# Performance work log

Hardware: AMD Instinct MI355X
Metric: run time of the kernel (lower is better)

## Reference

```python
import jax, jax.numpy as jnp
import numpy as np

EPS_NORM = 1e-12  # F.normalize eps
EPS_LN = 1e-5     # LayerNorm eps
TEMP = 0.1


def _l2norm(v, axis=-1):
    n = jnp.linalg.norm(v, axis=axis, keepdims=True)
    return v / jnp.maximum(n, EPS_NORM)


def setup_inputs() -> dict:
    key = jax.random.key(0)
    ks = jax.random.split(key, 6)
    B, D, P = 65536, 1024, 32
    x = jax.random.normal(ks[0], (B, D), dtype=jnp.float32)
    Wi = jax.random.normal(ks[1], (D, D), dtype=jnp.float32) * 0.02
    bi = jnp.zeros((D,), dtype=jnp.float32)
    Wo = jax.random.normal(ks[2], (D, 2 * D), dtype=jnp.float32) * 0.02
    bo = jnp.zeros((D,), dtype=jnp.float32)
    gamma = jnp.ones((D,), dtype=jnp.float32)
    beta = jnp.zeros((D,), dtype=jnp.float32)
    prototypes = _l2norm(jax.random.normal(ks[3], (P, D), dtype=jnp.float32))
    return {"x": x, "Wi": Wi, "bi": bi, "Wo": Wo, "bo": bo,
            "gamma": gamma, "beta": beta, "prototypes": prototypes}


def reference(x, Wi, bi, Wo, bo, gamma, beta, prototypes):
    # h = in_proj(x)
    h = x @ Wi.T + bi                      # [B, D]
    h_norm = _l2norm(h)
    proto_norm = _l2norm(prototypes)       # [P, D]
    sim = (h_norm @ proto_norm.T) / TEMP   # [B, P]
    attn = jax.nn.softmax(sim, axis=-1)
    retrieved = attn @ prototypes          # [B, D]
    combined = jnp.concatenate([x, retrieved], axis=-1)  # [B, 2D]
    out = jax.nn.gelu(combined @ Wo.T + bo, approximate=False)
    # dropout is identity in eval mode
    y = out + x
    mu = jnp.mean(y, axis=-1, keepdims=True)
    var = jnp.var(y, axis=-1, keepdims=True)
    return (y - mu) * jax.lax.rsqrt(var + EPS_LN) * gamma + beta
```

## Files before the change

### kernel.cpp

```cpp
#include <hip/hip_runtime.h>
#include <hip/hip_bf16.h>
#include <math.h>

typedef unsigned short u16;
typedef __attribute__((ext_vector_type(8))) short bf16x8;
typedef __attribute__((ext_vector_type(4))) float f32x4;
typedef __attribute__((address_space(1))) unsigned int gu32;
typedef __attribute__((address_space(3))) unsigned int lu32;

#define DD 1024
#define PP 32

__device__ __forceinline__ u16 f2bf(float f) {
  unsigned u = __float_as_uint(f);
  unsigned r = u + 0x7fffu + ((u >> 16) & 1u);
  return (u16)(r >> 16);
}
__device__ __forceinline__ float bf2f(u16 h) {
  return __uint_as_float(((unsigned)h) << 16);
}

__device__ __forceinline__ float gelu_t(float v) {
  float u = v + 0.044715f * v * v * v;
  float p = __builtin_amdgcn_exp2f(2.302590614f * u);
  float th = 1.0f - 2.0f * __builtin_amdgcn_rcpf(p + 1.0f);
  return 0.5f * v * (1.0f + th);
}

__global__ __launch_bounds__(256) void k_convert(const float* __restrict__ in,
                                                 u16* __restrict__ out, int n4) {
  for (int i = blockIdx.x * 256 + threadIdx.x; i < n4; i += gridDim.x * 256) {
    float4 v = ((const float4*)in)[i];
    ushort4 o;
    o.x = f2bf(v.x); o.y = f2bf(v.y); o.z = f2bf(v.z); o.w = f2bf(v.w);
    ((ushort4*)out)[i] = o;
  }
}

__global__ __launch_bounds__(256) void k_convert_wo(const float* __restrict__ Wo,
                                                    u16* __restrict__ WoB) {
  int i = blockIdx.x * 256 + threadIdx.x;
  int n = i >> 8, c4 = i & 255;
  float4 v = ((const float4*)(Wo + (size_t)n * 2048))[c4];
  ushort4 o;
  o.x = f2bf(v.x); o.y = f2bf(v.y); o.z = f2bf(v.z); o.w = f2bf(v.w);
  *(ushort4*)(WoB + (size_t)n * 1088 + c4 * 4) = o;
}

__global__ __launch_bounds__(256) void k_proto_prep(const float* __restrict__ protos,
                                                    u16* __restrict__ pb) {
  __shared__ float sb[4];
  int row = blockIdx.x, tid = threadIdx.x;
  float4 v = ((const float4*)(protos + row * DD))[tid];
  float q = v.x * v.x + v.y * v.y + v.z * v.z + v.w * v.w;
#pragma unroll
  for (int off = 32; off; off >>= 1) q += __shfl_xor(q, off);
  if ((tid & 63) == 0) sb[tid >> 6] = q;
  __syncthreads();
  q = sb[0] + sb[1] + sb[2] + sb[3];
  float inv = 1.0f / fmaxf(sqrtf(q), 1e-12f);
  ushort4 o;
  o.x = f2bf(v.x * inv); o.y = f2bf(v.y * inv); o.z = f2bf(v.z * inv); o.w = f2bf(v.w * inv);
  ((ushort4*)(pb + row * DD))[tid] = o;
}

__global__ __launch_bounds__(256) void k_p2(const float* __restrict__ Wo,
                                            const float* __restrict__ protos,
                                            u16* __restrict__ WoB) {
  __shared__ float swo[1024];
  int n = blockIdx.x, tid = threadIdx.x;
  ((float4*)swo)[tid] = ((const float4*)(Wo + (size_t)n * 2048 + 1024))[tid];
  __syncthreads();
  int w = tid >> 6, lane = tid & 63;
#pragma unroll
  for (int q = 0; q < 8; ++q) {
    int p = w * 8 + q;
    const float* pr = protos + (size_t)p * 1024 + lane * 16;
    const float* wv = swo + lane * 16;
    float d = 0.f;
#pragma unroll
    for (int j = 0; j < 16; ++j) d += wv[j] * pr[j];
#pragma unroll
    for (int off = 32; off; off >>= 1) d += __shfl_xor(d, off);
    if (lane == 0) WoB[(size_t)n * 1088 + 1024 + p] = f2bf(d);
  }
  if (tid < 32) WoB[(size_t)n * 1088 + 1056 + tid] = 0;
}

#define GLL(gsrc, ldst) __builtin_amdgcn_global_load_lds((gu32*)(gsrc), (lu32*)(ldst), 16, 0, 0)

template <int EPI, int NT>
__global__ __launch_bounds__(512, 2) void k_gemmF(const u16* __restrict__ A,
                                                  const u16* __restrict__ Aext,
                                                  const u16* __restrict__ Bm, int bstride,
                                                  const float* __restrict__ bias,
                                                  const u16* __restrict__ residb,
                                                  u16* __restrict__ Cout,
                                                  int nbn,
                                                  const u16* __restrict__ pbn,
                                                  float* __restrict__ simp,
                                                  float* __restrict__ ssp) {
  __shared__ u16 Lsh[65536];
#define ALS(bufv, idx) (Lsh + (bufv) * 16384 + (idx))
#define BLS(bufv, idx) (Lsh + 32768 + (bufv) * 16384 + (idx))
  const int tid = threadIdx.x;
  const int wid = tid >> 6, lane = tid & 63;
  const int wm = wid >> 2, wn = wid & 3;
  const int lm = lane & 15, lk = lane >> 4;

  const int scol_sw = (((lane & 7) ^ ((lane >> 3) & 7)) << 3);
  const int srow = lane >> 3;

  int g = blockIdx.x;
  int cpx = gridDim.x >> 3;
  int lin = (g & 7) * cpx + (g >> 3);
  int bn = lin % nbn, bm = lin / nbn;
  const size_t bmBase = (size_t)bm * 256;
  const size_t bnBase = (size_t)bn * 256;

  f32x4 acc[8][4];
#pragma unroll
  for (int i = 0; i < 8; ++i)
#pragma unroll
    for (int j = 0; j < 4; ++j) acc[i][j] = (f32x4){0.f, 0.f, 0.f, 0.f};

  bf16x8 a[4][2], b0[2][2], b1[2][2];

#define STAGE_A(bufv, kt, mh) do {                                              \
    int arow = (mh) * 64 + wid * 8 + srow;                                      \
    const u16 *ap0, *ap1;                                                       \
    if ((kt) < 16) {                                                            \
      ap0 = A + (bmBase + arow) * (size_t)1024 + scol_sw + (kt) * 64;           \
      ap1 = A + (bmBase + 128 + arow) * (size_t)1024 + scol_sw + (kt) * 64;     \
    } else {                                                                    \
      ap0 = Aext + (bmBase + arow) * (size_t)64 + scol_sw;                      \
      ap1 = Aext + (bmBase + 128 + arow) * (size_t)64 + scol_sw;                \
    }                                                                           \
    GLL(ap0, ALS(bufv, ((mh) * 64 + wid * 8) * 64));                            \
    GLL(ap1, ALS(bufv, (128 + (mh) * 64 + wid * 8) * 64));                      \
  } while (0)

#define STAGE_B(bufv, kt, nh) do {                                              \
    int br0 = ((wid >> 2) << 6) + (nh) * 32 + ((wid & 3) << 3);                 \
    int bcol = scol_sw + (kt) * 64;                                             \
    GLL(Bm + (bnBase + br0 + srow) * (size_t)bstride + bcol, BLS(bufv, br0 * 64)); \
    GLL(Bm + (bnBase + 128 + br0 + srow) * (size_t)bstride + bcol, BLS(bufv, (128 + br0) * 64)); \
  } while (0)

#define LOAD_A(bufv, mh) do {                                                   \
    _Pragma("unroll") for (int mi2 = 0; mi2 < 4; ++mi2) {                       \
      int row = wm * 128 + (mh) * 64 + mi2 * 16 + lm;                           \
      _Pragma("unroll") for (int kk = 0; kk < 2; ++kk)                          \
        a[mi2][kk] = *(const bf16x8*)ALS(bufv, row * 64 + ((kk * 32 + lk * 8) ^ ((lm & 7) << 3))); \
    }                                                                           \
  } while (0)

#define LOAD_B(dst, bufv, nh) do {                                              \
    _Pragma("unroll") for (int ni2 = 0; ni2 < 2; ++ni2) {                       \
      int row = wn * 64 + (nh) * 32 + ni2 * 16 + lm;                            \
      _Pragma("unroll") for (int kk = 0; kk < 2; ++kk)                          \
        dst[ni2][kk] = *(const bf16x8*)BLS(bufv, row * 64 + ((kk * 32 + lk * 8) ^ ((lm & 7) << 3))); \
    }                                                                           \
  } while (0)

#define BARRIER do { __builtin_amdgcn_s_barrier(); asm volatile("" ::: "memory"); } while (0)

#define MFMA_Q(bb, mh, nh) do {                                                 \
    __builtin_amdgcn_s_setprio(1);                                              \
    _Pragma("unroll") for (int mi2 = 0; mi2 < 4; ++mi2)                         \
    _Pragma("unroll") for (int ni2 = 0; ni2 < 2; ++ni2)                         \
    _Pragma("unroll") for (int kk = 0; kk < 2; ++kk)                            \
      acc[(mh) * 4 + mi2][(nh) * 2 + ni2] = __builtin_amdgcn_mfma_f32_16x16x32_bf16( \
          a[mi2][kk], bb[ni2][kk], acc[(mh) * 4 + mi2][(nh) * 2 + ni2], 0, 0, 0); \
    __builtin_amdgcn_s_setprio(0);                                              \
  } while (0)

#define TILE(T, P) do {                                                         \
    asm volatile("s_waitcnt vmcnt(0)" ::: "memory");                            \
    BARRIER;                                                                    \
    if ((T) + 1 < NT) {                                                         \
      STAGE_A((P) ^ 1, (T) + 1, 0); STAGE_B((P) ^ 1, (T) + 1, 0);               \
      STAGE_A((P) ^ 1, (T) + 1, 1); STAGE_B((P) ^ 1, (T) + 1, 1);               \
    }                                                                           \
    LOAD_A(P, 0); LOAD_B(b0, P, 0);                                             \
    MFMA_Q(b0, 0, 0);                                                           \
    LOAD_B(b1, P, 1);                                                           \
    MFMA_Q(b1, 0, 1);                                                           \
    LOAD_A(P, 1);                                                               \
    MFMA_Q(b1, 1, 1);                                                           \
    MFMA_Q(b0, 1, 0);                                                           \
  } while (0)

  STAGE_A(0, 0, 0); STAGE_B(0, 0, 0); STAGE_A(0, 0, 1); STAGE_B(0, 0, 1);

#pragma unroll
  for (int T = 0; T + 1 < NT; T += 2) {
    TILE(T, 0);
    TILE(T + 1, 1);
  }
  if (NT & 1) TILE(NT - 1, 0);

  __syncthreads();
  u16* eb = Lsh + wid * 4608;
  const size_t gr0 = bmBase + wm * 128;
  const int gc0 = (int)bnBase + wn * 64;

  if (EPI == 2) {
    bf16x8 bp[2][2];
#pragma unroll
    for (int ph = 0; ph < 2; ++ph)
#pragma unroll
      for (int kk = 0; kk < 2; ++kk)
        bp[ph][kk] = *(const bf16x8*)(pbn + (size_t)(ph * 16 + lm) * 1024 + gc0 + kk * 32 + lk * 8);
    f32x4 sa[2][4][2];
#pragma unroll
    for (int ch = 0; ch < 2; ++ch) {
#pragma unroll
      for (int mi2 = 0; mi2 < 4; ++mi2) {
        int mi = ch * 4 + mi2;
#pragma unroll
        for (int ni = 0; ni < 4; ++ni) {
          int col = ni * 16 + lm;
          float bv = bias[gc0 + ni * 16 + lm];
#pragma unroll
          for (int r = 0; r < 4; ++r) {
            int rowL = mi2 * 16 + lk * 4 + r;
            eb[rowL * 72 + (col ^ (((rowL >> 2) & 3) << 3))] = f2bf(acc[mi][ni][r] + bv);
          }
        }
      }
#pragma unroll
      for (int rg = 0; rg < 4; ++rg) {
        int rowL = rg * 16 + lm;
        int swz = ((lm >> 2) & 3) << 3;
        bf16x8 af0 = *(const bf16x8*)&eb[rowL * 72 + ((lk * 8) ^ swz)];
        bf16x8 af1 = *(const bf16x8*)&eb[rowL * 72 + ((32 + lk * 8) ^ swz)];
        float sq = 0.f;
#pragma unroll
        for (int j = 0; j < 8; ++j) {
          float h0 = bf2f((u16)af0[j]), h1 = bf2f((u16)af1[j]);
          sq += h0 * h0 + h1 * h1;
        }
        sq += __shfl_xor(sq, 16);
        sq += __shfl_xor(sq, 32);
        if (lk == 0)
          ssp[(gr0 + ch * 64 + rg * 16 + lm) * 16 + bn * 4 + wn] = sq;
        f32x4 z = {0.f, 0.f, 0.f, 0.f};
        f32x4 s0 = __builtin_amdgcn_mfma_f32_16x16x32_bf16(af0, bp[0][0], z, 0, 0, 0);
        s0 = __builtin_amdgcn_mfma_f32_16x16x32_bf16(af1, bp[0][1], s0, 0, 0, 0);
        f32x4 s1 = __builtin_amdgcn_mfma_f32_16x16x32_bf16(af0, bp[1][0], z, 0, 0, 0);
        s1 = __builtin_amdgcn_mfma_f32_16x16x32_bf16(af1, bp[1][1], s1, 0, 0, 0);
        sa[ch][rg][0] = s0;
        sa[ch][rg][1] = s1;
      }
    }
    __syncthreads();
    float* part = (float*)Lsh;
#pragma unroll
    for (int ch = 0; ch < 2; ++ch)
#pragma unroll
      for (int rg = 0; rg < 4; ++rg)
#pragma unroll
        for (int ph = 0; ph < 2; ++ph)
#pragma unroll
          for (int r = 0; r < 4; ++r) {
            int row = wm * 128 + ch * 64 + rg * 16 + lk * 4 + r;
            part[wn * 8192 + row * 32 + ph * 16 + lm] = sa[ch][rg][ph][r];
          }
    __syncthreads();
    for (int i = tid; i < 8192; i += 512) {
      int row = i >> 5, p = i & 31;
      float s = part[row * 32 + p] + part[8192 + row * 32 + p] +
                part[16384 + row * 32 + p] + part[24576 + row * 32 + p];
      simp[(bmBase + row) * 128 + (size_t)bn * 32 + p] = s;
    }
  } else {
#pragma unroll
    for (int ch = 0; ch < 2; ++ch) {
#pragma unroll
      for (int mi2 = 0; mi2 < 4; ++mi2) {
        int mi = ch * 4 + mi2;
#pragma unroll
        for (int ni = 0; ni < 4; ++ni) {
          int col = ni * 16 + lm;
          float bv = bias[gc0 + ni * 16 + lm];
#pragma unroll
          for (int r = 0; r < 4; ++r) {
            int rowL = mi2 * 16 + lk * 4 + r;
            float v = acc[mi][ni][r] + bv;
            v = gelu_t(v);
            eb[rowL * 72 + (col ^ (((rowL >> 2) & 3) << 3))] = f2bf(v);
          }
        }
      }
#pragma unroll
      for (int i = 0; i < 8; ++i) {
        int rowL = i * 8 + (lane >> 3);
        int c8 = (lane & 7) * 8;
        bf16x8 yv = *(const bf16x8*)&eb[rowL * 72 + (c8 ^ (((rowL >> 2) & 3) << 3))];
        size_t grow = gr0 + ch * 64 + rowL;
        bf16x8 rv = *(const bf16x8*)(residb + grow * 1024 + gc0 + c8);
        bf16x8 ov;
#pragma unroll
        for (int j = 0; j < 8; ++j)
          ov[j] = (short)f2bf(bf2f((u16)yv[j]) + bf2f((u16)rv[j]));
        *(bf16x8*)(Cout + grow * 2048 + gc0 + c8) = ov;
      }
    }
  }
#undef STAGE_A
#undef STAGE_B
#undef LOAD_A
#undef LOAD_B
#undef MFMA_Q
#undef TILE
#undef BARRIER
#undef ALS
#undef BLS
}

__global__ __launch_bounds__(256) void k_soft(const float* __restrict__ simp,
                                              const float* __restrict__ ssp,
                                              u16* __restrict__ ab) {
  const int wv = threadIdx.x >> 6, lane = threadIdx.x & 63;
  int rowBase = blockIdx.x * 32 + wv * 8;
#pragma unroll
  for (int i = 0; i < 8; ++i) {
    int row = rowBase + i;
    const float* sp = simp + (size_t)row * 128;
    float v = sp[lane] + sp[64 + lane];
    v += __shfl_xor(v, 32);
    float ssv = (lane < 16) ? ssp[(size_t)row * 16 + lane] : 0.f;
    ssv += __shfl_xor(ssv, 1); ssv += __shfl_xor(ssv, 2);
    ssv += __shfl_xor(ssv, 4); ssv += __shfl_xor(ssv, 8);
    float ss = __shfl(ssv, 0);
    float inv = 10.0f / fmaxf(sqrtf(ss), 1e-12f);
    float s = v * inv;
    float m = s;
#pragma unroll
    for (int off = 1; off < 32; off <<= 1) m = fmaxf(m, __shfl_xor(m, off));
    float e = expf(s - m);
    float sum = e;
#pragma unroll
    for (int off = 1; off < 32; off <<= 1) sum += __shfl_xor(sum, off);
    float a = e / sum;
    ab[(size_t)row * 64 + lane] = (lane < 32) ? f2bf(a) : (u16)0;
  }
}

__global__ __launch_bounds__(256) void k_ln2(u16* __restrict__ ybase,
                                             float* __restrict__ out,
                                             const float* __restrict__ gamma,
                                             const float* __restrict__ beta) {
  __shared__ float sb[8];
  size_t row = blockIdx.x;
  int tid = threadIdx.x;
  ushort4 v4 = ((const ushort4*)(ybase + row * 2048))[tid];
  float y0 = bf2f(v4.x), y1 = bf2f(v4.y), y2 = bf2f(v4.z), y3 = bf2f(v4.w);
  float s = y0 + y1 + y2 + y3;
  float q = y0 * y0 + y1 * y1 + y2 * y2 + y3 * y3;
#pragma unroll
  for (int off = 32; off; off >>= 1) { s += __shfl_xor(s, off); q += __shfl_xor(q, off); }
  if ((tid & 63) == 0) { sb[tid >> 6] = s; sb[4 + (tid >> 6)] = q; }
  __syncthreads();
  s = sb[0] + sb[1] + sb[2] + sb[3];
  q = sb[4] + sb[5] + sb[6] + sb[7];
  float mu = s * (1.f / 1024.f);
  float var = q * (1.f / 1024.f) - mu * mu;
  float rstd = rsqrtf(var + 1e-5f);
  float4 g = ((const float4*)gamma)[tid];
  float4 b = ((const float4*)beta)[tid];
  float4 o;
  o.x = (y0 - mu) * rstd * g.x + b.x;
  o.y = (y1 - mu) * rstd * g.y + b.y;
  o.z = (y2 - mu) * rstd * g.z + b.z;
  o.w = (y3 - mu) * rstd * g.w + b.w;
  ((float4*)(out + (row << 10)))[tid] = o;
}

extern "C" void kernel_launch(void* const* d_in, const int* in_sizes, int n_in,
                              void* d_out, int out_size, void* d_ws, size_t ws_size,
                              hipStream_t stream) {
  const float* x      = (const float*)d_in[0];
  const float* Wi     = (const float*)d_in[1];
  const float* bi     = (const float*)d_in[2];
  const float* Wo     = (const float*)d_in[3];
  const float* bo     = (const float*)d_in[4];
  const float* gamma  = (const float*)d_in[5];
  const float* beta   = (const float*)d_in[6];
  const float* protos = (const float*)d_in[7];
  const int Brows = in_sizes[0] / DD;

  u16* xb   = (u16*)d_ws;
  u16* WiB  = xb + (size_t)Brows * 1024;
  u16* WoB  = WiB + (size_t)1024 * 1024;
  u16* pb   = WoB + (size_t)1024 * 1088;
  u16* ab   = pb + (size_t)PP * DD;
  float* simp = (float*)(ab + (size_t)Brows * 64);
  float* ssp  = simp + (size_t)Brows * 128;
  u16* ybuf = (u16*)d_out;

  k_convert<<<4096, 256, 0, stream>>>(x, xb, Brows * 256);
  k_convert<<<1024, 256, 0, stream>>>(Wi, WiB, 1024 * 1024 / 4);
  k_convert_wo<<<1024, 256, 0, stream>>>(Wo, WoB);
  k_proto_prep<<<PP, 256, 0, stream>>>(protos, pb);
  k_p2<<<1024, 256, 0, stream>>>(Wo, protos, WoB);

  const int nbn = 1024 / 256;
  const int nwg = nbn * (Brows / 256);

  k_gemmF<2, 16><<<nwg, 512, 0, stream>>>(xb, xb, WiB, 1024, bi, nullptr,
                                          nullptr, nbn, pb, simp, ssp);
  k_soft<<<Brows / 32, 256, 0, stream>>>(simp, ssp, ab);
  k_gemmF<1, 17><<<nwg, 512, 0, stream>>>(xb, ab, WoB, 1088, bo, xb,
                                          ybuf, nbn, nullptr, nullptr, nullptr);
  k_ln2<<<Brows, 256, 0, stream>>>(ybuf, (float*)d_out, gamma, beta);
}
```

Before: 493.3 us.

## Switch GEMM inner loop to 32x32x16 MFMA tiles and fuse Wo conversion

Replaces the 16x16x32 bf16 MFMA tiling with 32x32x16 MFMAs, which changes the LDS fragment loads, the accumulator layout and the epilogue row/column mapping. This halves the number of MFMA instructions and fragment reads per K-step, cutting LDS traffic and issue overhead. It also folds the Wo bf16 conversion into the k_p2 kernel, removing one launch. Risks include reduced interleaving of loads with MFMAs, different register pressure, and mistakes in the new epilogue index mapping.

```diff
diff --git a/kernel.cpp b/kernel.cpp
--- a/kernel.cpp
+++ b/kernel.cpp
@@ -5,6 +5,7 @@
 typedef unsigned short u16;
 typedef __attribute__((ext_vector_type(8))) short bf16x8;
 typedef __attribute__((ext_vector_type(4))) float f32x4;
+typedef __attribute__((ext_vector_type(16))) float f32x16;
 typedef __attribute__((address_space(1))) unsigned int gu32;
 typedef __attribute__((address_space(3))) unsigned int lu32;
 
@@ -37,16 +38,6 @@
   }
 }
 
-__global__ __launch_bounds__(256) void k_convert_wo(const float* __restrict__ Wo,
-                                                    u16* __restrict__ WoB) {
-  int i = blockIdx.x * 256 + threadIdx.x;
-  int n = i >> 8, c4 = i & 255;
-  float4 v = ((const float4*)(Wo + (size_t)n * 2048))[c4];
-  ushort4 o;
-  o.x = f2bf(v.x); o.y = f2bf(v.y); o.z = f2bf(v.z); o.w = f2bf(v.w);
-  *(ushort4*)(WoB + (size_t)n * 1088 + c4 * 4) = o;
-}
-
 __global__ __launch_bounds__(256) void k_proto_prep(const float* __restrict__ protos,
                                                     u16* __restrict__ pb) {
   __shared__ float sb[4];
@@ -69,6 +60,10 @@
                                             u16* __restrict__ WoB) {
   __shared__ float swo[1024];
   int n = blockIdx.x, tid = threadIdx.x;
+  float4 lv = ((const float4*)(Wo + (size_t)n * 2048))[tid];
+  ushort4 lo;
+  lo.x = f2bf(lv.x); lo.y = f2bf(lv.y); lo.z = f2bf(lv.z); lo.w = f2bf(lv.w);
+  *(ushort4*)(WoB + (size_t)n * 1088 + tid * 4) = lo;
   ((float4*)swo)[tid] = ((const float4*)(Wo + (size_t)n * 2048 + 1024))[tid];
   __syncthreads();
   int w = tid >> 6, lane = tid & 63;
@@ -107,6 +102,7 @@
   const int wid = tid >> 6, lane = tid & 63;
   const int wm = wid >> 2, wn = wid & 3;
   const int lm = lane & 15, lk = lane >> 4;
+  const int l31 = lane & 31, l5 = lane >> 5;
 
   const int scol_sw = (((lane & 7) ^ ((lane >> 3) & 7)) << 3);
   const int srow = lane >> 3;
@@ -118,13 +114,15 @@
   const size_t bmBase = (size_t)bm * 256;
   const size_t bnBase = (size_t)bn * 256;
 
-  f32x4 acc[8][4];
-#pragma unroll
-  for (int i = 0; i < 8; ++i)
-#pragma unroll
-    for (int j = 0; j < 4; ++j) acc[i][j] = (f32x4){0.f, 0.f, 0.f, 0.f};
-
-  bf16x8 a[4][2], b0[2][2], b1[2][2];
+  f32x16 acc[4][2];
+#pragma unroll
+  for (int i = 0; i < 4; ++i)
+#pragma unroll
+    for (int j = 0; j < 2; ++j)
+#pragma unroll
+      for (int q = 0; q < 16; ++q) acc[i][j][q] = 0.f;
+
+  bf16x8 a[4][2], b[2][2];
 
 #define STAGE_A(bufv, kt, mh) do {                                              \
     int arow = (mh) * 64 + wid * 8 + srow;                                      \
@@ -147,31 +145,29 @@
     GLL(Bm + (bnBase + 128 + br0 + srow) * (size_t)bstride + bcol, BLS(bufv, (128 + br0) * 64)); \
   } while (0)
 
-#define LOAD_A(bufv, mh) do {                                                   \
-    _Pragma("unroll") for (int mi2 = 0; mi2 < 4; ++mi2) {                       \
-      int row = wm * 128 + (mh) * 64 + mi2 * 16 + lm;                           \
-      _Pragma("unroll") for (int kk = 0; kk < 2; ++kk)                          \
-        a[mi2][kk] = *(const bf16x8*)ALS(bufv, row * 64 + ((kk * 32 + lk * 8) ^ ((lm & 7) << 3))); \
+#define BARRIER do { __builtin_amdgcn_s_barrier(); asm volatile("" ::: "memory"); } while (0)
+
+#define KHALF(P, kh) do {                                                       \
+    _Pragma("unroll") for (int fm = 0; fm < 4; ++fm) {                          \
+      int row = wm * 128 + fm * 32 + l31;                                       \
+      _Pragma("unroll") for (int ks = 0; ks < 2; ++ks)                          \
+        a[fm][ks] = *(const bf16x8*)ALS(P, row * 64 +                           \
+            ((((kh) * 2 + ks) * 16 + l5 * 8) ^ ((l31 & 7) << 3)));              \
     }                                                                           \
-  } while (0)
-
-#define LOAD_B(dst, bufv, nh) do {                                              \
-    _Pragma("unroll") for (int ni2 = 0; ni2 < 2; ++ni2) {                       \
-      int row = wn * 64 + (nh) * 32 + ni2 * 16 + lm;                            \
-      _Pragma("unroll") for (int kk = 0; kk < 2; ++kk)                          \
-        dst[ni2][kk] = *(const bf16x8*)BLS(bufv, row * 64 + ((kk * 32 + lk * 8) ^ ((lm & 7) << 3))); \
+    _Pragma("unroll") for (int fn = 0; fn < 2; ++fn) {                          \
+      int row = wn * 64 + fn * 32 + l31;                                        \
+      _Pragma("unroll") for (int ks = 0; ks < 2; ++ks)                          \
+        b[fn][ks] = *(const bf16x8*)BLS(P, row * 64 +                           \
+            ((((kh) * 2 + ks) * 16 + l5 * 8) ^ ((l31 & 7) << 3)));              \
     }                                                                           \
-  } while (0)
-
-#define BARRIER do { __builtin_amdgcn_s_barrier(); asm volatile("" ::: "memory"); } while (0)
-
-#define MFMA_Q(bb, mh, nh) do {                                                 \
     __builtin_amdgcn_s_setprio(1);                                              \
-    _Pragma("unroll") for (int mi2 = 0; mi2 < 4; ++mi2)                         \
-    _Pragma("unroll") for (int ni2 = 0; ni2 < 2; ++ni2)                         \
-    _Pragma("unroll") for (int kk = 0; kk < 2; ++kk)                            \
-      acc[(mh) * 4 + mi2][(nh) * 2 + ni2] = __builtin_amdgcn_mfma_f32_16x16x32_bf16( \
-          a[mi2][kk], bb[ni2][kk], acc[(mh) * 4 + mi2][(nh) * 2 + ni2], 0, 0, 0); \
+    _Pragma("unroll") for (int fm = 0; fm < 4; ++fm)                            \
+    _Pragma("unroll") for (int fn = 0; fn < 2; ++fn) {                          \
+      acc[fm][fn] = __builtin_amdgcn_mfma_f32_32x32x16_bf16(                    \
+          a[fm][0], b[fn][0], acc[fm][fn], 0, 0, 0);                            \
+      acc[fm][fn] = __builtin_amdgcn_mfma_f32_32x32x16_bf16(                    \
+          a[fm][1], b[fn][1], acc[fm][fn], 0, 0, 0);                            \
+    }                                                                           \
     __builtin_amdgcn_s_setprio(0);                                              \
   } while (0)
 
@@ -182,13 +178,8 @@
       STAGE_A((P) ^ 1, (T) + 1, 0); STAGE_B((P) ^ 1, (T) + 1, 0);               \
       STAGE_A((P) ^ 1, (T) + 1, 1); STAGE_B((P) ^ 1, (T) + 1, 1);               \
     }                                                                           \
-    LOAD_A(P, 0); LOAD_B(b0, P, 0);                                             \
-    MFMA_Q(b0, 0, 0);                                                           \
-    LOAD_B(b1, P, 1);                                                           \
-    MFMA_Q(b1, 0, 1);                                                           \
-    LOAD_A(P, 1);                                                               \
-    MFMA_Q(b1, 1, 1);                                                           \
-    MFMA_Q(b0, 1, 0);                                                           \
+    KHALF(P, 0);                                                                \
+    KHALF(P, 1);                                                                \
   } while (0)
 
   STAGE_A(0, 0, 0); STAGE_B(0, 0, 0); STAGE_A(0, 0, 1); STAGE_B(0, 0, 1);
@@ -204,6 +195,9 @@
   u16* eb = Lsh + wid * 4608;
   const size_t gr0 = bmBase + wm * 128;
   const int gc0 = (int)bnBase + wn * 64;
+  float bv[2];
+  bv[0] = bias[gc0 + l31];
+  bv[1] = bias[gc0 + 32 + l31];
 
   if (EPI == 2) {
     bf16x8 bp[2][2];
@@ -216,16 +210,15 @@
 #pragma unroll
     for (int ch = 0; ch < 2; ++ch) {
 #pragma unroll
-      for (int mi2 = 0; mi2 < 4; ++mi2) {
-        int mi = ch * 4 + mi2;
-#pragma unroll
-        for (int ni = 0; ni < 4; ++ni) {
-          int col = ni * 16 + lm;
-          float bv = bias[gc0 + ni * 16 + lm];
-#pragma unroll
-          for (int r = 0; r < 4; ++r) {
-            int rowL = mi2 * 16 + lk * 4 + r;
-            eb[rowL * 72 + (col ^ (((rowL >> 2) & 3) << 3))] = f2bf(acc[mi][ni][r] + bv);
+      for (int fm2 = 0; fm2 < 2; ++fm2) {
+#pragma unroll
+        for (int fn = 0; fn < 2; ++fn) {
+#pragma unroll
+          for (int q = 0; q < 16; ++q) {
+            int rowL = fm2 * 32 + (q & 3) + ((q >> 2) << 3) + (l5 << 2);
+            int col = fn * 32 + l31;
+            eb[rowL * 72 + (col ^ (((rowL >> 2) & 3) << 3))] =
+                f2bf(acc[ch * 2 + fm2][fn][q] + bv[fn]);
           }
         }
       }
@@ -278,17 +271,14 @@
 #pragma unroll
     for (int ch = 0; ch < 2; ++ch) {
 #pragma unroll
-      for (int mi2 = 0; mi2 < 4; ++mi2) {
-        int mi = ch * 4 + mi2;
-#pragma unroll
-        for (int ni = 0; ni < 4; ++ni) {
-          int col = ni * 16 + lm;
-          float bv = bias[gc0 + ni * 16 + lm];
-#pragma unroll
-          for (int r = 0; r < 4; ++r) {
-            int rowL = mi2 * 16 + lk * 4 + r;
-            float v = acc[mi][ni][r] + bv;
-            v = gelu_t(v);
+      for (int fm2 = 0; fm2 < 2; ++fm2) {
+#pragma unroll
+        for (int fn = 0; fn < 2; ++fn) {
+#pragma unroll
+          for (int q = 0; q < 16; ++q) {
+            int rowL = fm2 * 32 + (q & 3) + ((q >> 2) << 3) + (l5 << 2);
+            int col = fn * 32 + l31;
+            float v = gelu_t(acc[ch * 2 + fm2][fn][q] + bv[fn]);
             eb[rowL * 72 + (col ^ (((rowL >> 2) & 3) << 3))] = f2bf(v);
           }
         }
@@ -310,9 +300,7 @@
   }
 #undef STAGE_A
 #undef STAGE_B
-#undef LOAD_A
-#undef LOAD_B
-#undef MFMA_Q
+#undef KHALF
 #undef TILE
 #undef BARRIER
 #undef ALS
@@ -402,7 +390,6 @@
 
   k_convert<<<4096, 256, 0, stream>>>(x, xb, Brows * 256);
   k_convert<<<1024, 256, 0, stream>>>(Wi, WiB, 1024 * 1024 / 4);
-  k_convert_wo<<<1024, 256, 0, stream>>>(Wo, WoB);
   k_proto_prep<<<PP, 256, 0, stream>>>(protos, pb);
   k_p2<<<1024, 256, 0, stream>>>(Wo, protos, WoB);
 
```

Measured after the change: 514.2 us. +4.2%, slower.
